# Optimization experiments

Hardware: AMD Instinct MI355X
Metric: run time of the kernel (lower is better)

The kernel has to match this reference:

```python
import jax, jax.numpy as jnp
import numpy as np

B, C, H, W, K = 2, 3, 256, 256, 51  # output H,W; filter size K; input is (H+K-1, W+K-1)


def _sepconv(inp, vertical, horizontal):
    # inp: [B,C,H+K-1,W+K-1]; vertical/horizontal: [B,K,H,W]
    Kf = vertical.shape[1]
    Ho, Wo = vertical.shape[2], vertical.shape[3]
    rows = jnp.stack([inp[:, :, i:i + Ho, :] for i in range(Kf)], axis=0)

    def body(acc, j):
        # window for horizontal offset j: [K,B,C,Ho,Wo]
        win = jax.lax.dynamic_slice_in_dim(rows, j, Wo, axis=4)
        # contract over vertical taps i with per-pixel vertical kernel
        vcon = jnp.einsum('kbchw,bkhw->bchw', win, vertical)
        # weight by per-pixel horizontal tap j and accumulate
        acc = acc + vcon * horizontal[:, j][:, None, :, :]
        return acc, None

    acc0 = jnp.zeros((inp.shape[0], inp.shape[1], Ho, Wo), inp.dtype)
    out, _ = jax.lax.scan(body, acc0, jnp.arange(Kf))
    return out


def setup_inputs() -> dict:
    key = jax.random.key(0)
    k1, k2, k3 = jax.random.split(key, 3)
    tenInput = jax.random.normal(k1, (B, C, H + K - 1, W + K - 1), dtype=jnp.float32)
    tenVertical = jax.random.normal(k2, (B, K, H, W), dtype=jnp.float32)
    tenHorizontal = jax.random.normal(k3, (B, K, H, W), dtype=jnp.float32)
    return {"tenInput": tenInput, "tenVertical": tenVertical, "tenHorizontal": tenHorizontal}


def reference(tenInput, tenVertical, tenHorizontal):
    return _sepconv(tenInput, tenVertical, tenHorizontal)
```

## Files before the change

### kernel.cpp

```cpp
#include <hip/hip_runtime.h>


namespace {
constexpr int KK = 51;
constexpr int NB = 2;
constexpr int NC = 3;
constexpr int HH = 256;
constexpr int WW = 256;
constexpr int IN_H = HH + KK - 1;
constexpr int IN_W = WW + KK - 1;

constexpr int TILE_W = 64;
constexpr int TILE_H = 8;
constexpr int NTX = 8;
constexpr int R = 8;
constexpr int NTY = 8;
constexpr int NS = 4;
constexpr int NTHREADS = NTX * NTY * NS;
constexpr int HALO_W = TILE_W + KK - 1;
constexpr int LDS_W = 116;
constexpr int LDS_H = 33;
constexpr int KSTRIDE = HH * WW;
constexpr int HCH = 4 * TILE_H * TILE_W;
constexpr int OUTN = NB * NC * HH * WW;
}

__device__ __forceinline__ float fget(const float4 v, int i) {
  return (i == 0) ? v.x : (i == 1) ? v.y : (i == 2) ? v.z : v.w;
}

template <int P, int JJ>
__device__ __forceinline__ void fma_jtap(const float4 (&v4)[4][2], const float4 (&w4)[4][3],
                                         const float4 ha, const float4 hb, float (&acc)[R]) {
#pragma unroll
  for (int rx = 0; rx < R; ++rx) {
    const int k  = rx + JJ;
    const int sl = (P + k / 4) % 3;
    const int cp = k & 3;
    const int vh = rx >> 2, vc = rx & 3;
    float tv = fget(v4[0][vh], vc) * fget(w4[0][sl], cp);
    tv = fmaf(fget(v4[1][vh], vc), fget(w4[1][sl], cp), tv);
    tv = fmaf(fget(v4[2][vh], vc), fget(w4[2][sl], cp), tv);
    tv = fmaf(fget(v4[3][vh], vc), fget(w4[3][sl], cp), tv);
    const float hv = (rx < 4) ? fget(ha, vc) : fget(hb, vc);
    acc[rx] = fmaf(hv, tv, acc[rx]);
  }
}

template <int P>
__device__ __forceinline__ void full_chunk(const float4 (&v4)[4][2], float4 (&w4)[4][3],
                                           const int (&woff)[4], int wcol,
                                           const float* hb, int off0, int off1,
                                           float (&acc)[R], const float* smem) {
  const float4 h0a = *reinterpret_cast<const float4*>(hb + off0);
  const float4 h0b = *reinterpret_cast<const float4*>(hb + off1);
  const float4 h1a = *reinterpret_cast<const float4*>(hb + 512 + off0);
  const float4 h1b = *reinterpret_cast<const float4*>(hb + 512 + off1);
  fma_jtap<P, 0>(v4, w4, h0a, h0b, acc);
  const float4 h2a = *reinterpret_cast<const float4*>(hb + 1024 + off0);
  const float4 h2b = *reinterpret_cast<const float4*>(hb + 1024 + off1);
  fma_jtap<P, 1>(v4, w4, h1a, h1b, acc);
  const float4 h3a = *reinterpret_cast<const float4*>(hb + 1536 + off0);
  const float4 h3b = *reinterpret_cast<const float4*>(hb + 1536 + off1);
  fma_jtap<P, 2>(v4, w4, h2a, h2b, acc);
  fma_jtap<P, 3>(v4, w4, h3a, h3b, acc);
#pragma unroll
  for (int ib = 0; ib < 4; ++ib)
    w4[ib][P] = *reinterpret_cast<const float4*>(&smem[woff[ib] + wcol]);
}

__global__ __launch_bounds__(NTHREADS, 1)
void sepconv_kernel(
    const float* __restrict__ inp,
    const float* __restrict__ vert,
    const float* __restrict__ horiz,
    float* __restrict__ ws)
{
  __shared__ float lds[LDS_H * LDS_W];
  __shared__ float hbuf[2 * HCH];

  const int tid = threadIdx.x;
  const int tx  = tid & (NTX - 1);
  const int ty  = (tid >> 3) & (NTY - 1);
  const int s   = tid >> 6;

  const int x0 = blockIdx.x * TILE_W;
  const int y0 = blockIdx.y * TILE_H;
  const int zz = blockIdx.z;
  const int bc = zz % (NB * NC);
  const int half = zz / (NB * NC);
  const int b  = bc / NC;
  const int c  = bc % NC;

  const int ROWBASE = half * 26;
  const int ROWMAX  = half ? 50 : 25;

  {
    const float* src = inp + (((size_t)(b * NC + c)) * IN_H) * IN_W + x0;
    constexpr int total2 = LDS_H * (HALO_W / 2);
    for (int e = tid; e < total2; e += NTHREADS) {
      const int col2 = e % (HALO_W / 2);
      const int r    = e / (HALO_W / 2);
      const int gr   = min(y0 + ROWBASE + r, IN_H - 1);
      const float2 v = *reinterpret_cast<const float2*>(src + (size_t)gr * IN_W + col2 * 2);
      float* dst = &lds[r * LDS_W + col2 * 2];
      dst[0] = v.x; dst[1] = v.y;
    }
  }

  const float* hblk = horiz + (((size_t)b * KK) * HH + y0) * WW + x0;
  int jj_[2], goff_[2], ldso_[2];
#pragma unroll
  for (int r = 0; r < 2; ++r) {
    const int p   = r * 256 + tid;
    const int rem = p & 127;
    const int row = rem >> 4;
    const int c4  = rem & 15;
    const int q   = (c4 - row) & 15;
    jj_[r]   = p >> 7;
    goff_[r] = row * WW + q * 4;
    ldso_[r] = (r * 256 + (tid & ~63)) * 4;
  }
  auto stage = [&](int cc, int bufn) {
#pragma unroll
    for (int r = 0; r < 2; ++r) {
      const int j  = 4 * cc + jj_[r];
      const int jc = (j <= 50) ? j : 50;
      const float* g = hblk + (size_t)jc * KSTRIDE + goff_[r];
      float* l = &hbuf[bufn * HCH + ldso_[r]];
      __builtin_amdgcn_global_load_lds((const __attribute__((address_space(1))) void*)g,
                                       (__attribute__((address_space(3))) void*)l, 16, 0, 0);
    }
  };

  stage(0, 0);
  __syncthreads();
  int buf = 0, ccn = 1;

  const int lx = tx * R;
  const int xg = x0 + lx;
  const int yg = y0 + ty;

  const int off0 = ty * 64 + ((2 * tx + ty) & 15) * 4;
  const int off1 = ty * 64 + ((2 * tx + 1 + ty) & 15) * 4;

  float acc[R];
#pragma unroll
  for (int rx = 0; rx < R; ++rx) acc[rx] = 0.f;

  const int blk0 = (s < 3) ? 2 * s : 6;
  const int nblk = (s < 3) ? 2 : 1;

  const float* vbase = vert + (((size_t)b * KK) * HH + yg) * WW + xg;

#pragma unroll 1
  for (int t = 0; t < 2; ++t) {
    const bool act = (t < nblk);
    float4 v4[4][2];
    float4 w4[4][3];
    int    woff[4];
    if (act) {
      const int ibase = ROWBASE + (blk0 + t) * 4;
#pragma unroll
      for (int ib = 0; ib < 4; ++ib) {
        const int iv = ibase + ib;
        const int ic = (iv <= ROWMAX) ? iv : ROWMAX;
        float4 va = *reinterpret_cast<const float4*>(vbase + (size_t)ic * KSTRIDE);
        float4 vb = *reinterpret_cast<const float4*>(vbase + (size_t)ic * KSTRIDE + 4);
        if (iv > ROWMAX) { va = make_float4(0.f, 0.f, 0.f, 0.f); vb = va; }
        v4[ib][0] = va; v4[ib][1] = vb;
        woff[ib] = (ty + ic - ROWBASE) * LDS_W;
        const float4* p = reinterpret_cast<const float4*>(&lds[woff[ib] + lx]);
        w4[ib][0] = p[0]; w4[ib][1] = p[1]; w4[ib][2] = p[2];
      }
    }

#pragma unroll 1
    for (int g = 0; g < 4; ++g) {
      const int base = lx + 12 * g + 12;
      stage(ccn, buf ^ 1); ccn = (ccn == 12) ? 0 : ccn + 1;
      if (act) full_chunk<0>(v4, w4, woff, base + 0, hbuf + buf * HCH, off0, off1, acc, lds);
      __syncthreads(); buf ^= 1;
      stage(ccn, buf ^ 1); ccn = (ccn == 12) ? 0 : ccn + 1;
      if (act) full_chunk<1>(v4, w4, woff, base + 4, hbuf + buf * HCH, off0, off1, acc, lds);
      __syncthreads(); buf ^= 1;
      stage(ccn, buf ^ 1); ccn = (ccn == 12) ? 0 : ccn + 1;
      if (act) full_chunk<2>(v4, w4, woff, base + 8, hbuf + buf * HCH, off0, off1, acc, lds);
      __syncthreads(); buf ^= 1;
    }

    stage(ccn, buf ^ 1); ccn = (ccn == 12) ? 0 : ccn + 1;
    if (act) {
      const float* hb = hbuf + buf * HCH;
      const float4 e0a = *reinterpret_cast<const float4*>(hb + off0);
      const float4 e0b = *reinterpret_cast<const float4*>(hb + off1);
      const float4 e1a = *reinterpret_cast<const float4*>(hb + 512 + off0);
      const float4 e1b = *reinterpret_cast<const float4*>(hb + 512 + off1);
      const float4 e2a = *reinterpret_cast<const float4*>(hb + 1024 + off0);
      const float4 e2b = *reinterpret_cast<const float4*>(hb + 1024 + off1);
      fma_jtap<0, 0>(v4, w4, e0a, e0b, acc);
      fma_jtap<0, 1>(v4, w4, e1a, e1b, acc);
      fma_jtap<0, 2>(v4, w4, e2a, e2b, acc);
    }
    __syncthreads(); buf ^= 1;
  }

  if (s > 0) {
    float* p = &lds[((s - 1) * 64 + ty * NTX + tx) * R];
#pragma unroll
    for (int rx = 0; rx < R; ++rx) p[rx] = acc[rx];
  }
  __syncthreads();
  if (s == 0) {
#pragma unroll
    for (int g = 0; g < 3; ++g) {
      const float* p = &lds[(g * 64 + ty * NTX + tx) * R];
#pragma unroll
      for (int rx = 0; rx < R; ++rx) acc[rx] += p[rx];
    }
    float* o = ws + (size_t)half * OUTN + (((size_t)(b * NC + c)) * HH + yg) * WW + xg;
    *reinterpret_cast<float4*>(o)     = make_float4(acc[0], acc[1], acc[2], acc[3]);
    *reinterpret_cast<float4*>(o + 4) = make_float4(acc[4], acc[5], acc[6], acc[7]);
  }
}

__global__ __launch_bounds__(256)
void sum_halves(const float4* __restrict__ a, const float4* __restrict__ b,
                float4* __restrict__ o)
{
  const int i = blockIdx.x * 256 + threadIdx.x;
  const float4 x = a[i], y = b[i];
  o[i] = make_float4(x.x + y.x, x.y + y.y, x.z + y.z, x.w + y.w);
}

extern "C" void kernel_launch(void* const* d_in, const int* in_sizes, int n_in,
                              void* d_out, int out_size, void* d_ws, size_t ws_size,
                              hipStream_t stream) {
  const float* inp   = (const float*)d_in[0];
  const float* vert  = (const float*)d_in[1];
  const float* horiz = (const float*)d_in[2];
  float* out = (float*)d_out;
  float* ws  = (float*)d_ws;

  dim3 grid(WW / TILE_W, HH / TILE_H, 2 * NB * NC);
  sepconv_kernel<<<grid, NTHREADS, 0, stream>>>(inp, vert, horiz, ws);

  const int n4 = OUTN / 4;
  sum_halves<<<n4 / 256, 256, 0, stream>>>(
      (const float4*)ws, (const float4*)(ws + OUTN), (float4*)out);
}
```

Measured before the change: 144.4 us.

## Give each wave its own horizontal-tap ring buffer and drop block barriers

```diff
diff --git a/kernel.cpp b/kernel.cpp
--- a/kernel.cpp
+++ b/kernel.cpp
@@ -21,7 +21,6 @@
 constexpr int LDS_W = 116;
 constexpr int LDS_H = 33;
 constexpr int KSTRIDE = HH * WW;
-constexpr int HCH = 4 * TILE_H * TILE_W;
 constexpr int OUTN = NB * NC * HH * WW;
 }
 
@@ -47,26 +46,13 @@
   }
 }
 
-template <int P>
-__device__ __forceinline__ void full_chunk(const float4 (&v4)[4][2], float4 (&w4)[4][3],
-                                           const int (&woff)[4], int wcol,
-                                           const float* hb, int off0, int off1,
-                                           float (&acc)[R], const float* smem) {
-  const float4 h0a = *reinterpret_cast<const float4*>(hb + off0);
-  const float4 h0b = *reinterpret_cast<const float4*>(hb + off1);
-  const float4 h1a = *reinterpret_cast<const float4*>(hb + 512 + off0);
-  const float4 h1b = *reinterpret_cast<const float4*>(hb + 512 + off1);
-  fma_jtap<P, 0>(v4, w4, h0a, h0b, acc);
-  const float4 h2a = *reinterpret_cast<const float4*>(hb + 1024 + off0);
-  const float4 h2b = *reinterpret_cast<const float4*>(hb + 1024 + off1);
-  fma_jtap<P, 1>(v4, w4, h1a, h1b, acc);
-  const float4 h3a = *reinterpret_cast<const float4*>(hb + 1536 + off0);
-  const float4 h3b = *reinterpret_cast<const float4*>(hb + 1536 + off1);
-  fma_jtap<P, 2>(v4, w4, h2a, h2b, acc);
-  fma_jtap<P, 3>(v4, w4, h3a, h3b, acc);
-#pragma unroll
-  for (int ib = 0; ib < 4; ++ib)
-    w4[ib][P] = *reinterpret_cast<const float4*>(&smem[woff[ib] + wcol]);
+template <int P, int JJ>
+__device__ __forceinline__ void chunk_fma(const float4 (&v4)[4][2], const float4 (&w4)[4][3],
+                                          const float* hb, int off0, int off1,
+                                          float (&acc)[R]) {
+  const float4 ha  = *reinterpret_cast<const float4*>(hb + off0);
+  const float4 hbv = *reinterpret_cast<const float4*>(hb + off1);
+  fma_jtap<P, JJ>(v4, w4, ha, hbv, acc);
 }
 
 __global__ __launch_bounds__(NTHREADS, 1)
@@ -77,12 +63,13 @@
     float* __restrict__ ws)
 {
   __shared__ float lds[LDS_H * LDS_W];
-  __shared__ float hbuf[2 * HCH];
-
-  const int tid = threadIdx.x;
-  const int tx  = tid & (NTX - 1);
-  const int ty  = (tid >> 3) & (NTY - 1);
-  const int s   = tid >> 6;
+  __shared__ float hbw[NS * 4 * 512];
+
+  const int tid  = threadIdx.x;
+  const int tx   = tid & (NTX - 1);
+  const int ty   = (tid >> 3) & (NTY - 1);
+  const int s    = tid >> 6;
+  const int lane = tid & 63;
 
   const int x0 = blockIdx.x * TILE_W;
   const int y0 = blockIdx.y * TILE_H;
@@ -109,33 +96,34 @@
   }
 
   const float* hblk = horiz + (((size_t)b * KK) * HH + y0) * WW + x0;
-  int jj_[2], goff_[2], ldso_[2];
+  int goffr[2];
 #pragma unroll
   for (int r = 0; r < 2; ++r) {
-    const int p   = r * 256 + tid;
-    const int rem = p & 127;
-    const int row = rem >> 4;
-    const int c4  = rem & 15;
-    const int q   = (c4 - row) & 15;
-    jj_[r]   = p >> 7;
-    goff_[r] = row * WW + q * 4;
-    ldso_[r] = (r * 256 + (tid & ~63)) * 4;
-  }
-  auto stage = [&](int cc, int bufn) {
-#pragma unroll
-    for (int r = 0; r < 2; ++r) {
-      const int j  = 4 * cc + jj_[r];
-      const int jc = (j <= 50) ? j : 50;
-      const float* g = hblk + (size_t)jc * KSTRIDE + goff_[r];
-      float* l = &hbuf[bufn * HCH + ldso_[r]];
-      __builtin_amdgcn_global_load_lds((const __attribute__((address_space(1))) void*)g,
-                                       (__attribute__((address_space(3))) void*)l, 16, 0, 0);
-    }
+    const int p   = r * 64 + lane;
+    const int row = p >> 4;
+    const int q   = ((p & 15) - row) & 15;
+    goffr[r] = row * WW + q * 4;
+  }
+  float* mybuf = &hbw[s * 2048];
+
+  int kStage = 0;
+  int jS     = 0;
+  auto stageK = [&]() {
+    const int j = (jS <= 50) ? jS : 50;
+    const float* g0 = hblk + (size_t)j * KSTRIDE;
+    float* dst = mybuf + (kStage & 3) * 512;
+#pragma unroll
+    for (int r = 0; r < 2; ++r)
+      __builtin_amdgcn_global_load_lds(
+          (const __attribute__((address_space(1))) void*)(g0 + goffr[r]),
+          (__attribute__((address_space(3))) void*)(dst + r * 256), 16, 0, 0);
+    ++kStage;
+    if (++jS == 52) jS = 0;
   };
 
-  stage(0, 0);
+  stageK(); stageK();
   __syncthreads();
-  int buf = 0, ccn = 1;
+  int kCur = 0;
 
   const int lx = tx * R;
   const int xg = x0 + lx;
@@ -153,58 +141,65 @@
 
   const float* vbase = vert + (((size_t)b * KK) * HH + yg) * WW + xg;
 
+#define CSTEP_PRE()                                                           \
+    asm volatile("s_waitcnt lgkmcnt(0)" ::: "memory");                        \
+    stageK();                                                                 \
+    asm volatile("s_waitcnt vmcnt(4)" ::: "memory");
+
+#define CSTEPN(PP, JJ)                                                        \
+  {                                                                           \
+    CSTEP_PRE();                                                              \
+    chunk_fma<PP, JJ>(v4, w4, mybuf + (kCur & 3) * 512, off0, off1, acc);     \
+    ++kCur;                                                                   \
+  }
+#define CSTEPR(PP, WCOL)                                                      \
+  {                                                                           \
+    CSTEP_PRE();                                                              \
+    chunk_fma<PP, 3>(v4, w4, mybuf + (kCur & 3) * 512, off0, off1, acc);      \
+    _Pragma("unroll")                                                         \
+    for (int ib = 0; ib < 4; ++ib)                                            \
+      w4[ib][PP] = *reinterpret_cast<const float4*>(&lds[woff[ib] + (WCOL)]); \
+    ++kCur;                                                                   \
+  }
+
 #pragma unroll 1
-  for (int t = 0; t < 2; ++t) {
-    const bool act = (t < nblk);
+  for (int t = 0; t < nblk; ++t) {
+    const int ibase = ROWBASE + (blk0 + t) * 4;
     float4 v4[4][2];
     float4 w4[4][3];
     int    woff[4];
-    if (act) {
-      const int ibase = ROWBASE + (blk0 + t) * 4;
-#pragma unroll
-      for (int ib = 0; ib < 4; ++ib) {
-        const int iv = ibase + ib;
-        const int ic = (iv <= ROWMAX) ? iv : ROWMAX;
-        float4 va = *reinterpret_cast<const float4*>(vbase + (size_t)ic * KSTRIDE);
-        float4 vb = *reinterpret_cast<const float4*>(vbase + (size_t)ic * KSTRIDE + 4);
-        if (iv > ROWMAX) { va = make_float4(0.f, 0.f, 0.f, 0.f); vb = va; }
-        v4[ib][0] = va; v4[ib][1] = vb;
-        woff[ib] = (ty + ic - ROWBASE) * LDS_W;
-        const float4* p = reinterpret_cast<const float4*>(&lds[woff[ib] + lx]);
-        w4[ib][0] = p[0]; w4[ib][1] = p[1]; w4[ib][2] = p[2];
-      }
+#pragma unroll
+    for (int ib = 0; ib < 4; ++ib) {
+      const int iv = ibase + ib;
+      const int ic = (iv <= ROWMAX) ? iv : ROWMAX;
+      float4 va = *reinterpret_cast<const float4*>(vbase + (size_t)ic * KSTRIDE);
+      float4 vb = *reinterpret_cast<const float4*>(vbase + (size_t)ic * KSTRIDE + 4);
+      if (iv > ROWMAX) { va = make_float4(0.f, 0.f, 0.f, 0.f); vb = va; }
+      v4[ib][0] = va; v4[ib][1] = vb;
+      woff[ib] = (ty + ic - ROWBASE) * LDS_W;
+      const float4* p = reinterpret_cast<const float4*>(&lds[woff[ib] + lx]);
+      w4[ib][0] = p[0]; w4[ib][1] = p[1]; w4[ib][2] = p[2];
     }
 
 #pragma unroll 1
-    for (int g = 0; g < 4; ++g) {
-      const int base = lx + 12 * g + 12;
-      stage(ccn, buf ^ 1); ccn = (ccn == 12) ? 0 : ccn + 1;
-      if (act) full_chunk<0>(v4, w4, woff, base + 0, hbuf + buf * HCH, off0, off1, acc, lds);
-      __syncthreads(); buf ^= 1;
-      stage(ccn, buf ^ 1); ccn = (ccn == 12) ? 0 : ccn + 1;
-      if (act) full_chunk<1>(v4, w4, woff, base + 4, hbuf + buf * HCH, off0, off1, acc, lds);
-      __syncthreads(); buf ^= 1;
-      stage(ccn, buf ^ 1); ccn = (ccn == 12) ? 0 : ccn + 1;
-      if (act) full_chunk<2>(v4, w4, woff, base + 8, hbuf + buf * HCH, off0, off1, acc, lds);
-      __syncthreads(); buf ^= 1;
-    }
-
-    stage(ccn, buf ^ 1); ccn = (ccn == 12) ? 0 : ccn + 1;
-    if (act) {
-      const float* hb = hbuf + buf * HCH;
-      const float4 e0a = *reinterpret_cast<const float4*>(hb + off0);
-      const float4 e0b = *reinterpret_cast<const float4*>(hb + off1);
-      const float4 e1a = *reinterpret_cast<const float4*>(hb + 512 + off0);
-      const float4 e1b = *reinterpret_cast<const float4*>(hb + 512 + off1);
-      const float4 e2a = *reinterpret_cast<const float4*>(hb + 1024 + off0);
-      const float4 e2b = *reinterpret_cast<const float4*>(hb + 1024 + off1);
-      fma_jtap<0, 0>(v4, w4, e0a, e0b, acc);
-      fma_jtap<0, 1>(v4, w4, e1a, e1b, acc);
-      fma_jtap<0, 2>(v4, w4, e2a, e2b, acc);
-    }
-    __syncthreads(); buf ^= 1;
-  }
-
+    for (int g2 = 0; g2 < 4; ++g2) {
+      const int cb = lx + 12 * g2 + 12;
+      CSTEPN(0, 0); CSTEPN(0, 1); CSTEPN(0, 2); CSTEPR(0, cb + 0);
+      CSTEPN(1, 0); CSTEPN(1, 1); CSTEPN(1, 2); CSTEPR(1, cb + 4);
+      CSTEPN(2, 0); CSTEPN(2, 1); CSTEPN(2, 2); CSTEPR(2, cb + 8);
+    }
+    CSTEPN(0, 0); CSTEPN(0, 1); CSTEPN(0, 2);
+    {
+      asm volatile("s_waitcnt lgkmcnt(0)" ::: "memory");
+      stageK();
+      ++kCur;
+    }
+  }
+#undef CSTEPN
+#undef CSTEPR
+#undef CSTEP_PRE
+
+  __syncthreads();
   if (s > 0) {
     float* p = &lds[((s - 1) * 64 + ty * NTX + tx) * R];
 #pragma unroll
```

Result: slower. 182.9 us (+26.6%).
